# Kernel optimization log

Hardware: AMD Instinct MI355X
Metric: run time of the kernel (lower is better)

## Reference

```python
import jax, jax.numpy as jnp
import numpy as np

NEG_INF = -9.0e15  # matches torch's -9000000000000000.0 mask value
ALPHA = 0.2        # LeakyReLU negative slope


def setup_inputs() -> dict:
    key = jax.random.key(0)
    k1, k2, k3, k4 = jax.random.split(key, 4)
    N, F_in, F_out = 8192, 128, 128
    x = jax.random.normal(k1, (N, F_in), dtype=jnp.float32)
    adj = jax.random.randint(k2, (N, N), 0, 2, dtype=jnp.int32)
    W = jax.random.normal(k3, (F_in, F_out), dtype=jnp.float32) * (1.0 / np.sqrt(F_in))
    a = jax.random.normal(k4, (2 * F_out, 1), dtype=jnp.float32) * (1.0 / np.sqrt(2 * F_out))
    return {"x": x, "adj": adj, "W": W, "a": a}


def reference(x, adj, W, a):
    # h = W(input): [N, F_out]
    h = x @ W
    F_out = h.shape[1]
    # a([h_i || h_j]) = h_i . a[:F] + h_j . a[F:]  -- identical math to the
    # original NxNx2F concat, without materializing it.
    a_src = a[:F_out, 0]   # coefficients on the row (i) node
    a_dst = a[F_out:, 0]   # coefficients on the column (j) node
    s_src = h @ a_src      # [N]
    s_dst = h @ a_dst      # [N]
    e = jax.nn.leaky_relu(s_src[:, None] + s_dst[None, :], negative_slope=ALPHA)  # [N, N]
    e = jnp.where(adj > 0, e, jnp.float32(NEG_INF))
    attention = jax.nn.softmax(e, axis=1)
    # dropout omitted (identity at eval) for a deterministic baseline
    h_prime = attention @ h  # [N, F_out]
    return h_prime
```

## Files before the change

kernel.cpp:

```cpp
#include <hip/hip_runtime.h>

#define N 8192
#define F 128
#define ALPHA 0.2f

typedef __attribute__((ext_vector_type(8))) short short8;
typedef __attribute__((ext_vector_type(4))) float f32x4;
typedef unsigned short u16;

__device__ __forceinline__ u16 f2bf(float f) {
    unsigned int u = __float_as_uint(f);
    u += 0x7fff + ((u >> 16) & 1);
    return (u16)(u >> 16);
}

__global__ __launch_bounds__(256) void gemm_h(const float* __restrict__ x,
                                              const float* __restrict__ W,
                                              const float* __restrict__ aa,
                                              u16* __restrict__ hT,
                                              float* __restrict__ ssrc,
                                              float* __restrict__ sdst) {
    __shared__ float xs[32 * 128];
    __shared__ float Wsh[32 * 128];
    const int t = threadIdx.x;
    const int i0 = blockIdx.x * 32;
    const int c4 = (t & 31) * 4;
    const int r8 = t >> 5;

#pragma unroll
    for (int p = 0; p < 4; ++p) {
        int rr = p * 8 + r8;
        *(float4*)&xs[rr * 128 + c4] = *(const float4*)&x[(size_t)(i0 + rr) * 128 + c4];
    }

    const int tx = t & 31, ty = t >> 5;
    const int r0 = ty * 4, c0 = tx * 4;
    float acc[4][4] = {};

    for (int kc = 0; kc < 4; ++kc) {
        __syncthreads();
#pragma unroll
        for (int p = 0; p < 4; ++p) {
            int k = p * 8 + r8;
            *(float4*)&Wsh[k * 128 + c4] = *(const float4*)&W[(kc * 32 + k) * 128 + c4];
        }
        __syncthreads();
#pragma unroll 4
        for (int k = 0; k < 32; k += 4) {
            float xr[4][4];
#pragma unroll
            for (int rr = 0; rr < 4; ++rr)
                *(float4*)xr[rr] = *(const float4*)&xs[(r0 + rr) * 128 + kc * 32 + k];
#pragma unroll
            for (int kk = 0; kk < 4; ++kk) {
                float4 wv = *(const float4*)&Wsh[(k + kk) * 128 + c0];
#pragma unroll
                for (int rr = 0; rr < 4; ++rr) {
                    acc[rr][0] += xr[rr][kk] * wv.x;
                    acc[rr][1] += xr[rr][kk] * wv.y;
                    acc[rr][2] += xr[rr][kk] * wv.z;
                    acc[rr][3] += xr[rr][kk] * wv.w;
                }
            }
        }
    }

#pragma unroll
    for (int rr = 0; rr < 4; ++rr)
#pragma unroll
        for (int cc = 0; cc < 4; ++cc)
            hT[(size_t)(c0 + cc) * N + (i0 + r0 + rr)] = f2bf(acc[rr][cc]);

    float4 asv = *(const float4*)&aa[c0];
    float4 adv = *(const float4*)&aa[F + c0];
#pragma unroll
    for (int rr = 0; rr < 4; ++rr) {
        float vs = acc[rr][0] * asv.x + acc[rr][1] * asv.y + acc[rr][2] * asv.z + acc[rr][3] * asv.w;
        float vd = acc[rr][0] * adv.x + acc[rr][1] * adv.y + acc[rr][2] * adv.z + acc[rr][3] * adv.w;
#pragma unroll
        for (int off = 16; off >= 1; off >>= 1) {
            vs += __shfl_down(vs, off, 32);
            vd += __shfl_down(vd, off, 32);
        }
        if (tx == 0) {
            ssrc[i0 + r0 + rr] = vs;
            sdst[i0 + r0 + rr] = vd;
        }
    }
}

__global__ __launch_bounds__(256, 2) void attn_fused(const int* __restrict__ adj,
                                                     const u16* __restrict__ hT,
                                                     const float* __restrict__ ssrc,
                                                     const float* __restrict__ sdst,
                                                     float* __restrict__ out) {
    __shared__ float accsh[4][16][132];
    __shared__ float srow[4][16];

    const int t = threadIdx.x;
    const int w = t >> 6, L = t & 63;
    const int quad = L >> 4, l16 = L & 15;
    const int tile0 = blockIdx.x * 16;
    const int prow = tile0 + l16;
    const int JW = N / 4;
    const int jbase = w * JW;
    const int NC = JW / 32;

    const float s_i = ssrc[prow];
    const int* pA = adj + (size_t)prow * N + jbase + quad * 8;
    const float* pD = sdst + jbase + quad * 8;
    const u16* pB = hT + (size_t)l16 * N + jbase + quad * 8;

    f32x4 acc[8];
#pragma unroll
    for (int cg = 0; cg < 8; ++cg) acc[cg] = 0.f;
    float rsum = 0.f;

    auto mk_frag = [&](int4 a0, int4 a1, float4 d0, float4 d1) -> short8 {
        const int m[8] = {a0.x, a0.y, a0.z, a0.w, a1.x, a1.y, a1.z, a1.w};
        const float d[8] = {d0.x, d0.y, d0.z, d0.w, d1.x, d1.y, d1.z, d1.w};
        float wv[8];
#pragma unroll
        for (int k = 0; k < 8; ++k) {
            float z = s_i + d[k];
            float e = __expf(fmaxf(z, ALPHA * z));
            wv[k] = (m[k] > 0) ? e : 0.f;
        }
        union { unsigned int u[4]; short8 s8; } pk;
        float s = 0.f;
#pragma unroll
        for (int p = 0; p < 4; ++p) {
            unsigned int r;
            asm("v_cvt_pk_bf16_f32 %0, %1, %2" : "=v"(r) : "v"(wv[2 * p]), "v"(wv[2 * p + 1]));
            pk.u[p] = r;
            s += __uint_as_float(r << 16);
            s += __uint_as_float(r & 0xffff0000u);
        }
        rsum += s;
        return pk.s8;
    };

    int4 A0x = *(const int4*)(pA);       int4 A0y = *(const int4*)(pA + 4);
    int4 A1x = *(const int4*)(pA + 32);  int4 A1y = *(const int4*)(pA + 36);
    int4 A2x = *(const int4*)(pA + 64);  int4 A2y = *(const int4*)(pA + 68);
    int4 A3x = *(const int4*)(pA + 96);  int4 A3y = *(const int4*)(pA + 100);
    float4 D0x = *(const float4*)(pD);      float4 D0y = *(const float4*)(pD + 4);
    float4 D1x = *(const float4*)(pD + 32); float4 D1y = *(const float4*)(pD + 36);

    short8 Bbuf[8];
#pragma unroll
    for (int cg = 0; cg < 8; ++cg)
        Bbuf[cg] = *(const short8*)(pB + (size_t)cg * 16 * N);

    for (int c = 0; c < NC; ++c) {
        const int cb = (c + 1 < NC) ? c + 1 : NC - 1;
        short8 Bload[8];
#pragma unroll
        for (int cg = 0; cg < 8; ++cg)
            Bload[cg] = *(const short8*)(pB + (size_t)cg * 16 * N + cb * 32);

        const int ca = (c + 4 < NC) ? c + 4 : NC - 1;
        const int cd = (c + 2 < NC) ? c + 2 : NC - 1;
        int4 nAx = *(const int4*)(pA + ca * 32);
        int4 nAy = *(const int4*)(pA + ca * 32 + 4);
        float4 nDx = *(const float4*)(pD + cd * 32);
        float4 nDy = *(const float4*)(pD + cd * 32 + 4);

        short8 af = mk_frag(A0x, A0y, D0x, D0y);

#pragma unroll
        for (int cg = 0; cg < 8; ++cg)
            acc[cg] = __builtin_amdgcn_mfma_f32_16x16x32_bf16(af, Bbuf[cg], acc[cg], 0, 0, 0);

        A0x = A1x; A0y = A1y;
        A1x = A2x; A1y = A2y;
        A2x = A3x; A2y = A3y;
        A3x = nAx; A3y = nAy;
        D0x = D1x; D0y = D1y;
        D1x = nDx; D1y = nDy;
#pragma unroll
        for (int cg = 0; cg < 8; ++cg) Bbuf[cg] = Bload[cg];
    }

    rsum += __shfl_xor(rsum, 16);
    rsum += __shfl_xor(rsum, 32);
    if (L < 16) srow[w][l16] = rsum;

#pragma unroll
    for (int cg = 0; cg < 8; ++cg)
#pragma unroll
        for (int r = 0; r < 4; ++r)
            accsh[w][quad * 4 + r][cg * 16 + l16] = acc[cg][r];

    __syncthreads();

#pragma unroll
    for (int p = 0; p < 2; ++p) {
        const int fid = t * 2 + p;
        const int row = fid >> 5;
        const int c4 = (fid & 31) * 4;
        float4 s0 = *(const float4*)&accsh[0][row][c4];
        float4 s1 = *(const float4*)&accsh[1][row][c4];
        float4 s2 = *(const float4*)&accsh[2][row][c4];
        float4 s3 = *(const float4*)&accsh[3][row][c4];
        const float inv = 1.0f / (srow[0][row] + srow[1][row] + srow[2][row] + srow[3][row]);
        float4 o = {(s0.x + s1.x + s2.x + s3.x) * inv,
                    (s0.y + s1.y + s2.y + s3.y) * inv,
                    (s0.z + s1.z + s2.z + s3.z) * inv,
                    (s0.w + s1.w + s2.w + s3.w) * inv};
        *(float4*)&out[(size_t)(tile0 + row) * F + c4] = o;
    }
}

extern "C" void kernel_launch(void* const* d_in, const int* in_sizes, int n_in,
                              void* d_out, int out_size, void* d_ws, size_t ws_size,
                              hipStream_t stream) {
    (void)in_sizes; (void)n_in; (void)out_size; (void)ws_size;
    const float* x   = (const float*)d_in[0];
    const int*   adj = (const int*)d_in[1];
    const float* W   = (const float*)d_in[2];
    const float* a   = (const float*)d_in[3];
    float* out = (float*)d_out;

    u16* hT     = (u16*)d_ws;
    float* ssrc = (float*)(hT + (size_t)N * F);
    float* sdst = ssrc + N;

    gemm_h<<<N / 32, 256, 0, stream>>>(x, W, a, hT, ssrc, sdst);
    attn_fused<<<N / 16, 256, 0, stream>>>(adj, hT, ssrc, sdst, out);
}
```

Before: 484.7 us.

## Stream adj and hT tiles into LDS via async global_load_lds double buffering

Replaces the register-held prefetch pipelines for the adjacency mask and the bf16 hT operand with per-wave, double-buffered direct global-to-LDS loads (global_load_lds). Each iteration issues the next chunk's loads, waits with an explicit vmcnt, then reads fragments back from LDS. The aim is to cut VGPR pressure from the deep register prefetch and let loads overlap compute asynchronously. In exchange, the adj prefetch distance shrinks from four chunks to one. LDS use also grows to 80KB per block, reused for the final reduction, which relies on two blocks per CU fitting in LDS.

```diff
diff --git a/kernel.cpp b/kernel.cpp
--- a/kernel.cpp
+++ b/kernel.cpp
@@ -89,13 +89,20 @@
     }
 }
 
+#define WAITVM(n) asm volatile("s_waitcnt vmcnt(" #n ")" ::: "memory")
+
+__device__ __forceinline__ void dma16(const void* g, void* l) {
+    __builtin_amdgcn_global_load_lds(
+        (const __attribute__((address_space(1))) unsigned int*)g,
+        (__attribute__((address_space(3))) unsigned int*)l, 16, 0, 0);
+}
+
 __global__ __launch_bounds__(256, 2) void attn_fused(const int* __restrict__ adj,
                                                      const u16* __restrict__ hT,
                                                      const float* __restrict__ ssrc,
                                                      const float* __restrict__ sdst,
                                                      float* __restrict__ out) {
-    __shared__ float accsh[4][16][132];
-    __shared__ float srow[4][16];
+    __shared__ __align__(16) char ldsraw[4 * 20480];
 
     const int t = threadIdx.x;
     const int w = t >> 6, L = t & 63;
@@ -106,6 +113,8 @@
     const int jbase = w * JW;
     const int NC = JW / 32;
 
+    char* ldsw = ldsraw + w * 20480;
+
     const float s_i = ssrc[prow];
     const int* pA = adj + (size_t)prow * N + jbase + quad * 8;
     const float* pD = sdst + jbase + quad * 8;
@@ -140,57 +149,63 @@
         return pk.s8;
     };
 
-    int4 A0x = *(const int4*)(pA);       int4 A0y = *(const int4*)(pA + 4);
-    int4 A1x = *(const int4*)(pA + 32);  int4 A1y = *(const int4*)(pA + 36);
-    int4 A2x = *(const int4*)(pA + 64);  int4 A2y = *(const int4*)(pA + 68);
-    int4 A3x = *(const int4*)(pA + 96);  int4 A3y = *(const int4*)(pA + 100);
-    float4 D0x = *(const float4*)(pD);      float4 D0y = *(const float4*)(pD + 4);
-    float4 D1x = *(const float4*)(pD + 32); float4 D1y = *(const float4*)(pD + 36);
-
-    short8 Bbuf[8];
-#pragma unroll
-    for (int cg = 0; cg < 8; ++cg)
-        Bbuf[cg] = *(const short8*)(pB + (size_t)cg * 16 * N);
-
+    auto issue_chunk = [&](int cc, int b) {
+        const int coff = cc * 32;
+        char* base = ldsw + b * 10240;
+#pragma unroll
+        for (int cg = 0; cg < 8; ++cg)
+            dma16(pB + (size_t)cg * 16 * N + coff, base + cg * 1024);
+        dma16(pA + coff, base + 8192);
+        dma16(pA + coff + 4, base + 9216);
+    };
+
+    issue_chunk(0, 0);
+    float4 D0x = *(const float4*)(pD);
+    float4 D0y = *(const float4*)(pD + 4);
+    float4 D1x = *(const float4*)(pD + 32);
+    float4 D1y = *(const float4*)(pD + 36);
+
+#pragma unroll 1
     for (int c = 0; c < NC; ++c) {
         const int cb = (c + 1 < NC) ? c + 1 : NC - 1;
-        short8 Bload[8];
-#pragma unroll
-        for (int cg = 0; cg < 8; ++cg)
-            Bload[cg] = *(const short8*)(pB + (size_t)cg * 16 * N + cb * 32);
-
-        const int ca = (c + 4 < NC) ? c + 4 : NC - 1;
+        issue_chunk(cb, (c + 1) & 1);
         const int cd = (c + 2 < NC) ? c + 2 : NC - 1;
-        int4 nAx = *(const int4*)(pA + ca * 32);
-        int4 nAy = *(const int4*)(pA + ca * 32 + 4);
         float4 nDx = *(const float4*)(pD + cd * 32);
         float4 nDy = *(const float4*)(pD + cd * 32 + 4);
 
-        short8 af = mk_frag(A0x, A0y, D0x, D0y);
-
+        WAITVM(12);
+        __builtin_amdgcn_sched_barrier(0);
+
+        const char* bb = ldsw + (c & 1) * 10240;
+        int4 a0 = *(const int4*)(bb + 8192 + (size_t)L * 16);
+        int4 a1 = *(const int4*)(bb + 9216 + (size_t)L * 16);
+        short8 Bv[8];
 #pragma unroll
         for (int cg = 0; cg < 8; ++cg)
-            acc[cg] = __builtin_amdgcn_mfma_f32_16x16x32_bf16(af, Bbuf[cg], acc[cg], 0, 0, 0);
-
-        A0x = A1x; A0y = A1y;
-        A1x = A2x; A1y = A2y;
-        A2x = A3x; A2y = A3y;
-        A3x = nAx; A3y = nAy;
-        D0x = D1x; D0y = D1y;
-        D1x = nDx; D1y = nDy;
-#pragma unroll
-        for (int cg = 0; cg < 8; ++cg) Bbuf[cg] = Bload[cg];
-    }
+            Bv[cg] = *(const short8*)(bb + cg * 1024 + (size_t)L * 16);
+
+        short8 af = mk_frag(a0, a1, D0x, D0y);
+#pragma unroll
+        for (int cg = 0; cg < 8; ++cg)
+            acc[cg] = __builtin_amdgcn_mfma_f32_16x16x32_bf16(af, Bv[cg], acc[cg], 0, 0, 0);
+
+        D0x = D1x; D0y = D1y; D1x = nDx; D1y = nDy;
+    }
+
+    WAITVM(0);
+    __builtin_amdgcn_sched_barrier(0);
 
     rsum += __shfl_xor(rsum, 16);
     rsum += __shfl_xor(rsum, 32);
-    if (L < 16) srow[w][l16] = rsum;
+    float* acw = (float*)ldsw;
+    float* srw = (float*)(ldsw + 8448);
+    if (L < 16) srw[l16] = rsum;
 
 #pragma unroll
     for (int cg = 0; cg < 8; ++cg)
 #pragma unroll
         for (int r = 0; r < 4; ++r)
-            accsh[w][quad * 4 + r][cg * 16 + l16] = acc[cg][r];
+            acw[(quad * 4 + r) * 132 + cg * 16 + l16] = acc[cg][r];
 
     __syncthreads();
 
@@ -199,15 +214,17 @@
         const int fid = t * 2 + p;
         const int row = fid >> 5;
         const int c4 = (fid & 31) * 4;
-        float4 s0 = *(const float4*)&accsh[0][row][c4];
-        float4 s1 = *(const float4*)&accsh[1][row][c4];
-        float4 s2 = *(const float4*)&accsh[2][row][c4];
-        float4 s3 = *(const float4*)&accsh[3][row][c4];
-        const float inv = 1.0f / (srow[0][row] + srow[1][row] + srow[2][row] + srow[3][row]);
-        float4 o = {(s0.x + s1.x + s2.x + s3.x) * inv,
-                    (s0.y + s1.y + s2.y + s3.y) * inv,
-                    (s0.z + s1.z + s2.z + s3.z) * inv,
-                    (s0.w + s1.w + s2.w + s3.w) * inv};
+        float inv = 0.f;
+        float4 o = {0.f, 0.f, 0.f, 0.f};
+#pragma unroll
+        for (int wv = 0; wv < 4; ++wv) {
+            const float* aw = (const float*)(ldsraw + wv * 20480);
+            float4 s = *(const float4*)&aw[row * 132 + c4];
+            o.x += s.x; o.y += s.y; o.z += s.z; o.w += s.w;
+            inv += ((const float*)(ldsraw + wv * 20480 + 8448))[row];
+        }
+        inv = 1.0f / inv;
+        o.x *= inv; o.y *= inv; o.z *= inv; o.w *= inv;
         *(float4*)&out[(size_t)(tile0 + row) * F + c4] = o;
     }
 }
```

After: 484.8 us. About the same (+0.0%).
